# Kernel tuning notes

Measured on AMD Instinct MI355X. Metric: run time of the kernel, lower is better.

The kernel has to match this reference:

```python
import jax, jax.numpy as jnp
import numpy as np

B, S, H, KVH, D = 1, 2048, 32, 8, 128
ROPE_THETA = 500000.0


def _rotate_half(x):
    x1, x2 = jnp.split(x, 2, axis=-1)
    return jnp.concatenate((-x2, x1), axis=-1)


def setup_inputs() -> dict:
    key = jax.random.key(0)
    ks = jax.random.split(key, 5)
    hidden_states = jax.random.normal(ks[0], (B, S, H * D), dtype=jnp.float32)
    Wq = jax.random.normal(ks[1], (H * D, H * D), dtype=jnp.float32) * 0.02
    Wk = jax.random.normal(ks[2], (KVH * D, H * D), dtype=jnp.float32) * 0.02
    Wv = jax.random.normal(ks[3], (KVH * D, H * D), dtype=jnp.float32) * 0.02
    Wo = jax.random.normal(ks[4], (H * D, H * D), dtype=jnp.float32) * 0.02
    # rotary tables (Llama-style, concat of freqs with itself)
    inv_freq = 1.0 / (ROPE_THETA ** (jnp.arange(0, D, 2, dtype=jnp.float32) / D))
    freqs = jnp.arange(S, dtype=jnp.float32)[:, None] * inv_freq[None, :]  # [S, D/2]
    emb = jnp.concatenate((freqs, freqs), axis=-1)  # [S, D]
    cos = jnp.cos(emb)[None]  # [1, S, D]
    sin = jnp.sin(emb)[None]
    # additive causal mask, matching SDPA attn_mask semantics
    causal = jnp.tril(jnp.ones((S, S), dtype=bool))
    attention_mask = jnp.where(causal, 0.0, -1e9).astype(jnp.float32)[None, None]  # [1,1,S,S]
    return {"hidden_states": hidden_states, "attention_mask": attention_mask,
            "cos": cos, "sin": sin, "Wq": Wq, "Wk": Wk, "Wv": Wv, "Wo": Wo}


def reference(hidden_states, attention_mask, cos, sin, Wq, Wk, Wv, Wo):
    b, s, _ = hidden_states.shape
    d = cos.shape[-1]
    h = Wq.shape[0] // d
    kvh = Wk.shape[0] // d
    g = h // kvh  # GQA group size

    # fused QKV projection (nn.Linear: y = x @ W^T), then split heads -> [b, heads, s, d]
    q = jnp.einsum('bsi,oi->bso', hidden_states, Wq).reshape(b, s, h, d).transpose(0, 2, 1, 3)
    k = jnp.einsum('bsi,oi->bso', hidden_states, Wk).reshape(b, s, kvh, d).transpose(0, 2, 1, 3)
    v = jnp.einsum('bsi,oi->bso', hidden_states, Wv).reshape(b, s, kvh, d).transpose(0, 2, 1, 3)

    # rotary embedding (unsqueeze_dim=1)
    c = cos[:, None]  # [b,1,s,d]
    sn = sin[:, None]
    q = q * c + _rotate_half(q) * sn
    k = k * c + _rotate_half(k) * sn

    # GQA: view q as [b, kvh, g, s, d]; contract against un-repeated k/v
    qg = q.reshape(b, kvh, g, s, d)
    scale = 1.0 / jnp.sqrt(jnp.float32(d))
    scores = jnp.einsum('bkgsd,bktd->bkgst', qg, k) * scale  # [b,kvh,g,s,s]
    scores = scores + attention_mask[:, :, None]  # broadcast [b,1,1,s,s]
    probs = jax.nn.softmax(scores, axis=-1)
    attn = jnp.einsum('bkgst,bktd->bkgsd', probs, v)  # [b,kvh,g,s,d]

    attn = attn.reshape(b, h, s, d).transpose(0, 2, 1, 3).reshape(b, s, h * d)
    out = jnp.einsum('bso,po->bsp', attn, Wo)
    return out
```

## Files before the change

### kernel.cpp

```cpp
#include <hip/hip_runtime.h>
#include <hip/hip_bf16.h>

#define SEQ 2048
#define HD  128
#define NH  32
#define NKV 8
#define MODEL 4096
#define KVDIM 1024
#define QKVN 6144

typedef __attribute__((ext_vector_type(8))) short short8;
typedef __attribute__((ext_vector_type(4))) short short4v;
typedef __attribute__((ext_vector_type(4))) float float4v;

#define MFMA16(a, b, c) __builtin_amdgcn_mfma_f32_16x16x32_bf16(a, b, c, 0, 0, 0)

__device__ __forceinline__ short f2bf(float x) {
  unsigned u = __builtin_bit_cast(unsigned, x);
  u += 0x7fffu + ((u >> 16) & 1u);
  return (short)(u >> 16);
}
__device__ __forceinline__ float bf2f(short s) {
  unsigned u = ((unsigned)(unsigned short)s) << 16;
  return __builtin_bit_cast(float, u);
}

__device__ __forceinline__ void async_copy16(const void* g, void* l) {
  __builtin_amdgcn_global_load_lds((const __attribute__((address_space(1))) void*)g,
                                   (__attribute__((address_space(3))) void*)l, 16, 0, 0);
}

__global__ __launch_bounds__(256) void cast_bf16(const float* __restrict__ in,
                                                 short* __restrict__ out, int n) {
  int i = (blockIdx.x * 256 + threadIdx.x) * 4;
  if (i < n) {
    float4v v = *(const float4v*)(in + i);
    short4v o;
    o[0] = f2bf(v[0]); o[1] = f2bf(v[1]); o[2] = f2bf(v[2]); o[3] = f2bf(v[3]);
    *(short4v*)(out + i) = o;
  }
}

__device__ __forceinline__ void store_out(float* C, size_t idx, float v) { C[idx] = v; }
__device__ __forceinline__ void store_out(short* C, size_t idx, float v) { C[idx] = f2bf(v); }

template <int NI, typename OUT>
__global__ __launch_bounds__(512, 2) void gemm256v(const short* __restrict__ A,
                                                   const short* __restrict__ B,
                                                   OUT* __restrict__ C,
                                                   int M, int N, int K) {
  constexpr int BN = NI * 64;
  __shared__ __align__(16) short As[2][256 * 64];
  __shared__ __align__(16) short Bs[2][BN * 64];
  const int tid = threadIdx.x;
  const int lane = tid & 63, w = tid >> 6;
  const int col = lane & 15, quad = lane >> 4;
  const int wm = w >> 2, wn = w & 3;

  const int nbx = N / BN;
  int bid = blockIdx.x, nwg = gridDim.x;
  int swz = (nwg & 7) ? bid : ((bid & 7) * (nwg >> 3) + (bid >> 3));
  const int m0 = (swz / nbx) << 8;
  const int n0 = (swz % nbx) * BN;

  const int srow = tid >> 3;
  const int schunk = (tid & 7) ^ (srow & 7);
  const short* pA = A + (size_t)(m0 + srow) * K + schunk * 8;
  const short* pB = B + (size_t)(n0 + srow) * K + schunk * 8;
  const int ldst = tid * 8;

  const int sw = (col & 7) << 3;
  const int kof0 = (quad * 8) ^ sw;
  const int kof1 = (32 + quad * 8) ^ sw;
  const int ra = wm * 128, rb = wn * (NI * 16);

  float4v acc[8][NI] = {};
  const int iters = K >> 6;

#define SA(buf, rA, kt) async_copy16(pA + (size_t)(rA) * K + (kt), &As[buf][(rA) * 64 + ldst])
#define SB_(buf, rB, kt) async_copy16(pB + (size_t)(rB) * K + (kt), &Bs[buf][(rB) * 64 + ldst])

  SA(0, 0, 0);  SA(0, 128, 0);
  SB_(0, 0, 0); SB_(0, 64, 0);
  if constexpr (NI == 3) SB_(0, 128, 0);
  SA(0, 64, 0); SA(0, 192, 0);
  asm volatile("s_waitcnt vmcnt(2)" ::: "memory");
  __builtin_amdgcn_s_barrier();

  for (int t = 0; t < iters; ++t) {
    const int cb = t & 1, nb = cb ^ 1;
    const int kt = (t + 1) << 6;
    const bool pf = (t + 1 < iters);
    const short* a_ = As[cb];
    const short* b_ = Bs[cb];
    short8 bf[NI][2];
    short8 af[2][2];

#pragma unroll
    for (int j = 0; j < 2; ++j) {
      const short* rp = a_ + (ra + j * 16 + col) * 64;
      af[j][0] = *(const short8*)(rp + kof0);
      af[j][1] = *(const short8*)(rp + kof1);
    }
#pragma unroll
    for (int ni = 0; ni < NI; ++ni) {
      const short* rp = b_ + (rb + ni * 16 + col) * 64;
      bf[ni][0] = *(const short8*)(rp + kof0);
      bf[ni][1] = *(const short8*)(rp + kof1);
    }
    if (pf) { SA(nb, 0, kt); SA(nb, 128, kt); }
    __builtin_amdgcn_s_barrier();
    asm volatile("s_waitcnt lgkmcnt(0)" ::: "memory");
    __builtin_amdgcn_sched_barrier(0);
    __builtin_amdgcn_s_setprio(1);
#pragma unroll
    for (int j = 0; j < 2; ++j)
#pragma unroll
      for (int ni = 0; ni < NI; ++ni) {
        acc[j][ni] = MFMA16(af[j][0], bf[ni][0], acc[j][ni]);
        acc[j][ni] = MFMA16(af[j][1], bf[ni][1], acc[j][ni]);
      }
    __builtin_amdgcn_s_setprio(0);
    __builtin_amdgcn_s_barrier();

#pragma unroll
    for (int j = 0; j < 2; ++j) {
      const short* rp = a_ + (ra + (2 + j) * 16 + col) * 64;
      af[j][0] = *(const short8*)(rp + kof0);
      af[j][1] = *(const short8*)(rp + kof1);
    }
    if (pf) { SB_(nb, 0, kt); SB_(nb, 64, kt); }
    __builtin_amdgcn_s_barrier();
    asm volatile("s_waitcnt lgkmcnt(0)" ::: "memory");
    __builtin_amdgcn_sched_barrier(0);
    __builtin_amdgcn_s_setprio(1);
#pragma unroll
    for (int j = 0; j < 2; ++j)
#pragma unroll
      for (int ni = 0; ni < NI; ++ni) {
        acc[2 + j][ni] = MFMA16(af[j][0], bf[ni][0], acc[2 + j][ni]);
        acc[2 + j][ni] = MFMA16(af[j][1], bf[ni][1], acc[2 + j][ni]);
      }
    __builtin_amdgcn_s_setprio(0);
    if (pf) asm volatile("s_waitcnt vmcnt(4)" ::: "memory");
    else    asm volatile("s_waitcnt vmcnt(0)" ::: "memory");
    __builtin_amdgcn_s_barrier();

#pragma unroll
    for (int j = 0; j < 2; ++j) {
      const short* rp = a_ + (ra + (4 + j) * 16 + col) * 64;
      af[j][0] = *(const short8*)(rp + kof0);
      af[j][1] = *(const short8*)(rp + kof1);
    }
    if (pf) { if constexpr (NI == 3) SB_(nb, 128, kt); }
    __builtin_amdgcn_s_barrier();
    asm volatile("s_waitcnt lgkmcnt(0)" ::: "memory");
    __builtin_amdgcn_sched_barrier(0);
    __builtin_amdgcn_s_setprio(1);
#pragma unroll
    for (int j = 0; j < 2; ++j)
#pragma unroll
      for (int ni = 0; ni < NI; ++ni) {
        acc[4 + j][ni] = MFMA16(af[j][0], bf[ni][0], acc[4 + j][ni]);
        acc[4 + j][ni] = MFMA16(af[j][1], bf[ni][1], acc[4 + j][ni]);
      }
    __builtin_amdgcn_s_setprio(0);
    __builtin_amdgcn_s_barrier();

#pragma unroll
    for (int j = 0; j < 2; ++j) {
      const short* rp = a_ + (ra + (6 + j) * 16 + col) * 64;
      af[j][0] = *(const short8*)(rp + kof0);
      af[j][1] = *(const short8*)(rp + kof1);
    }
    if (pf) { SA(nb, 64, kt); SA(nb, 192, kt); }
    __builtin_amdgcn_s_barrier();
    asm volatile("s_waitcnt lgkmcnt(0)" ::: "memory");
    __builtin_amdgcn_sched_barrier(0);
    __builtin_amdgcn_s_setprio(1);
#pragma unroll
    for (int j = 0; j < 2; ++j)
#pragma unroll
      for (int ni = 0; ni < NI; ++ni) {
        acc[6 + j][ni] = MFMA16(af[j][0], bf[ni][0], acc[6 + j][ni]);
        acc[6 + j][ni] = MFMA16(af[j][1], bf[ni][1], acc[6 + j][ni]);
      }
    __builtin_amdgcn_s_setprio(0);
    if (pf) asm volatile("s_waitcnt vmcnt(2)" ::: "memory");
    __builtin_amdgcn_s_barrier();
  }
#undef SA
#undef SB_

#pragma unroll
  for (int mi = 0; mi < 8; ++mi)
#pragma unroll
    for (int ni = 0; ni < NI; ++ni)
#pragma unroll
      for (int r = 0; r < 4; ++r) {
        int row = m0 + ra + mi * 16 + quad * 4 + r;
        int cc  = n0 + rb + ni * 16 + col;
        store_out(C, (size_t)row * N + cc, acc[mi][ni][r]);
      }
}

__global__ __launch_bounds__(128) void rope_kernel(const short* __restrict__ qkv,
                                                   const float* __restrict__ cosp,
                                                   const float* __restrict__ sinp,
                                                   short* __restrict__ qb,
                                                   short* __restrict__ kb) {
  int s = blockIdx.x, head = blockIdx.y, d = threadIdx.x;
  float c  = cosp[s * HD + d];
  float sn = sinp[s * HD + d];
  if (head < NH) {
    const short* base = qkv + (size_t)s * QKVN + head * HD;
    float x = bf2f(base[d]);
    float rot = (d < 64) ? -bf2f(base[d + 64]) : bf2f(base[d - 64]);
    qb[((size_t)(head * SEQ + s)) * HD + d] = f2bf((x * c + rot * sn) * 0.08838834764831845f);
  } else {
    int hk = head - NH;
    const short* base = qkv + (size_t)s * QKVN + MODEL + hk * HD;
    float x = bf2f(base[d]);
    float rot = (d < 64) ? -bf2f(base[d + 64]) : bf2f(base[d - 64]);
    kb[((size_t)(hk * SEQ + s)) * HD + d] = f2bf(x * c + rot * sn);
  }
}

__global__ __launch_bounds__(256) void vtrans_kernel(const short* __restrict__ qkv,
                                                     short* __restrict__ vt) {
  __shared__ short tile[32][34];
  int kv = blockIdx.z;
  int d0 = blockIdx.x * 32, s0 = blockIdx.y * 32;
  int tx = threadIdx.x, ty = threadIdx.y;
#pragma unroll
  for (int j = 0; j < 32; j += 8)
    tile[ty + j][tx] = qkv[(size_t)(s0 + ty + j) * QKVN + MODEL + KVDIM + kv * HD + d0 + tx];
  __syncthreads();
#pragma unroll
  for (int j = 0; j < 32; j += 8)
    vt[((size_t)(kv * HD + d0 + ty + j)) * SEQ + s0 + tx] = tile[tx][ty + j];
}

#define FKT 32
#define KLD 136
#define VLD 40
#define PLD 40

__global__ __launch_bounds__(256, 3) void flash_attn(const short* __restrict__ qb_,
                                                     const short* __restrict__ kb,
                                                     const short* __restrict__ vt,
                                                     short* __restrict__ attn) {
  __shared__ __align__(16) short Ks[2][FKT * KLD];
  __shared__ __align__(16) short Vs[2][HD * VLD];
  __shared__ __align__(16) short Ps[4][32 * PLD];
  const int tid = threadIdx.x;
  const int w = tid >> 6, lane = tid & 63;
  const int col = lane & 15, quad = lane >> 4;
  const int h = blockIdx.x;
  const int kv = h >> 2;
  const int yp = (blockIdx.y < 8) ? (15 - (int)blockIdx.y) : ((int)blockIdx.y - 8);
  const int qB0 = yp * 128;
  const int q0w = qB0 + w * 32;
  const int ntiles = qB0 / FKT + 4;

  short8 ones;
#pragma unroll
  for (int i = 0; i < 8; i++) ones[i] = (short)0x3F80;

  short8 qf[2][4];
  const short* qbase = qb_ + ((size_t)(h * SEQ + q0w + col)) * HD;
#pragma unroll
  for (int rt = 0; rt < 2; rt++)
#pragma unroll
    for (int ks = 0; ks < 4; ks++)
      qf[rt][ks] = *(const short8*)(qbase + rt * 16 * HD + ks * 32 + quad * 8);

  float4v o[2][8] = {};
  float4v la[2] = {};

  const int kg_off = tid * 8;
  const int klds0  = (kg_off >> 7) * KLD + (kg_off & 127);
  const int vd     = tid >> 2;
  const int vkof   = (tid & 3) * 8;
  const size_t vrow0 = ((size_t)(kv * HD + vd)) * SEQ;
  const size_t vrow1 = ((size_t)(kv * HD + vd + 64)) * SEQ;
  const int vlds0 = vd * VLD + vkof;
  const short* kgbase = kb + ((size_t)kv * SEQ) * HD;

  short8 kr0, kr1, vr0, vr1;
  kr0 = *(const short8*)(kgbase + kg_off);
  kr1 = *(const short8*)(kgbase + 2048 + kg_off);
  vr0 = *(const short8*)(vt + vrow0 + vkof);
  vr1 = *(const short8*)(vt + vrow1 + vkof);
  *(short8*)&Ks[0][klds0]            = kr0;
  *(short8*)&Ks[0][klds0 + 16 * KLD] = kr1;
  *(short8*)&Vs[0][vlds0]            = vr0;
  *(short8*)&Vs[0][vlds0 + 64 * VLD] = vr1;
  __syncthreads();

  for (int kt = 0; kt < ntiles; kt++) {
    const int b = kt & 1;
    const int key0 = kt * FKT;
    if (kt + 1 < ntiles) {
      const int nk0 = key0 + FKT;
      const short* kg = kgbase + (size_t)nk0 * HD;
      kr0 = *(const short8*)(kg + kg_off);
      kr1 = *(const short8*)(kg + 2048 + kg_off);
      vr0 = *(const short8*)(vt + vrow0 + nk0 + vkof);
      vr1 = *(const short8*)(vt + vrow1 + nk0 + vkof);
    }
    if (key0 <= q0w + 31) {
      float4v sct[2][2] = {};
#pragma unroll
      for (int ks = 0; ks < 4; ks++) {
        short8 kf0 = *(const short8*)&Ks[b][col * KLD + ks * 32 + quad * 8];
        short8 kf1 = *(const short8*)&Ks[b][(16 + col) * KLD + ks * 32 + quad * 8];
        sct[0][0] = MFMA16(kf0, qf[0][ks], sct[0][0]);
        sct[0][1] = MFMA16(kf0, qf[1][ks], sct[0][1]);
        sct[1][0] = MFMA16(kf1, qf[0][ks], sct[1][0]);
        sct[1][1] = MFMA16(kf1, qf[1][ks], sct[1][1]);
      }
      short* pw = Ps[w];
#pragma unroll
      for (int rt = 0; rt < 2; rt++) {
        int qrow = q0w + rt * 16 + col;
#pragma unroll
        for (int kt2 = 0; kt2 < 2; kt2++) {
          int keyb = key0 + kt2 * 16 + quad * 4;
          short4v p;
#pragma unroll
          for (int r = 0; r < 4; r++) {
            float s = sct[kt2][rt][r];
            if (keyb + r > qrow) s = -INFINITY;
            p[r] = f2bf(__expf(s));
          }
          *(short4v*)&pw[(rt * 16 + col) * PLD + kt2 * 16 + quad * 4] = p;
        }
      }
      asm volatile("s_waitcnt lgkmcnt(0)" ::: "memory");
      short8 pf0 = *(const short8*)&pw[col * PLD + quad * 8];
      short8 pf1 = *(const short8*)&pw[(16 + col) * PLD + quad * 8];
      la[0] = MFMA16(ones, pf0, la[0]);
      la[1] = MFMA16(ones, pf1, la[1]);
#pragma unroll
      for (int nc = 0; nc < 8; nc++) {
        short8 vb = *(const short8*)&Vs[b][(nc * 16 + col) * VLD + quad * 8];
        o[0][nc] = MFMA16(vb, pf0, o[0][nc]);
        o[1][nc] = MFMA16(vb, pf1, o[1][nc]);
      }
    }
    if (kt + 1 < ntiles) {
      const int nb = 1 - b;
      *(short8*)&Ks[nb][klds0]            = kr0;
      *(short8*)&Ks[nb][klds0 + 16 * KLD] = kr1;
      *(short8*)&Vs[nb][vlds0]            = vr0;
      *(short8*)&Vs[nb][vlds0 + 64 * VLD] = vr1;
    }
    __syncthreads();
  }

#pragma unroll
  for (int rt = 0; rt < 2; rt++) {
    float inv = 1.0f / la[rt][0];
    size_t rowbase = (size_t)(q0w + rt * 16 + col) * MODEL + h * HD + quad * 4;
#pragma unroll
    for (int nc = 0; nc < 8; nc++) {
      short4v ov;
#pragma unroll
      for (int r = 0; r < 4; r++) ov[r] = f2bf(o[rt][nc][r] * inv);
      *(short4v*)(attn + rowbase + nc * 16) = ov;
    }
  }
}

extern "C" void kernel_launch(void* const* d_in, const int* in_sizes, int n_in,
                              void* d_out, int out_size, void* d_ws, size_t ws_size,
                              hipStream_t stream) {
  const float* hidden = (const float*)d_in[0];
  const float* cosp = (const float*)d_in[2];
  const float* sinp = (const float*)d_in[3];
  const float* Wq   = (const float*)d_in[4];
  const float* Wk   = (const float*)d_in[5];
  const float* Wv   = (const float*)d_in[6];
  const float* Wo   = (const float*)d_in[7];

  char* ws = (char*)d_ws;
  size_t off = 0;
  auto alloc = [&](size_t bytes) {
    char* p = ws + off;
    off += (bytes + 255) & ~(size_t)255;
    return p;
  };
  short* wq_bf = (short*)alloc((size_t)MODEL * MODEL * 2);
  short* wk_bf = (short*)alloc((size_t)KVDIM * MODEL * 2);
  short* wv_bf = (short*)alloc((size_t)KVDIM * MODEL * 2);
  short* wo_bf = (short*)alloc((size_t)MODEL * MODEL * 2);
  short* h_bf  = (short*)alloc((size_t)SEQ * MODEL * 2);
  short* qkv_bf = (short*)alloc((size_t)SEQ * QKVN * 2);
  short* k_bf  = (short*)alloc((size_t)NKV * SEQ * HD * 2);
  short* v_t   = (short*)alloc((size_t)NKV * HD * SEQ * 2);
  short* attn_bf = (short*)alloc((size_t)SEQ * MODEL * 2);
  short* q_bf    = h_bf;

  {
    int n;
    n = SEQ * MODEL;    cast_bf16<<<n / 1024, 256, 0, stream>>>(hidden, h_bf, n);
    n = MODEL * MODEL;  cast_bf16<<<n / 1024, 256, 0, stream>>>(Wq, wq_bf, n);
    n = KVDIM * MODEL;  cast_bf16<<<n / 1024, 256, 0, stream>>>(Wk, wk_bf, n);
    n = KVDIM * MODEL;  cast_bf16<<<n / 1024, 256, 0, stream>>>(Wv, wv_bf, n);
    n = MODEL * MODEL;  cast_bf16<<<n / 1024, 256, 0, stream>>>(Wo, wo_bf, n);
  }

  gemm256v<3, short><<<dim3((SEQ / 256) * (QKVN / 192)), 512, 0, stream>>>(
      h_bf, wq_bf, qkv_bf, SEQ, QKVN, MODEL);

  rope_kernel<<<dim3(SEQ, NH + NKV), 128, 0, stream>>>(qkv_bf, cosp, sinp, q_bf, k_bf);
  vtrans_kernel<<<dim3(HD / 32, SEQ / 32, NKV), dim3(32, 8), 0, stream>>>(qkv_bf, v_t);

  flash_attn<<<dim3(NH, SEQ / 128), 256, 0, stream>>>(q_bf, k_bf, v_t, attn_bf);

  gemm256v<2, float><<<dim3((SEQ / 256) * (MODEL / 128)), 512, 0, stream>>>(
      attn_bf, wo_bf, (float*)d_out, SEQ, MODEL, MODEL);
}
```

Before: 542.6 us.

## Fuse input casts, restructure GEMM phases, add 128x128 GEMM for output projection

```diff
diff --git a/kernel.cpp b/kernel.cpp
--- a/kernel.cpp
+++ b/kernel.cpp
@@ -30,22 +30,32 @@
                                    (__attribute__((address_space(3))) void*)l, 16, 0, 0);
 }
 
-__global__ __launch_bounds__(256) void cast_bf16(const float* __restrict__ in,
-                                                 short* __restrict__ out, int n) {
-  int i = (blockIdx.x * 256 + threadIdx.x) * 4;
-  if (i < n) {
-    float4v v = *(const float4v*)(in + i);
-    short4v o;
-    o[0] = f2bf(v[0]); o[1] = f2bf(v[1]); o[2] = f2bf(v[2]); o[3] = f2bf(v[3]);
-    *(short4v*)(out + i) = o;
-  }
+__global__ __launch_bounds__(256) void cast_fused(const float* __restrict__ wq,
+                                                  const float* __restrict__ wk,
+                                                  const float* __restrict__ wv,
+                                                  const float* __restrict__ wo,
+                                                  const float* __restrict__ hid,
+                                                  short* __restrict__ dst) {
+  int b = blockIdx.x;
+  const float* src;
+  int rbase, lblk;
+  if (b < 16384)      { src = wq;  rbase = 0;     lblk = b; }
+  else if (b < 20480) { src = wk;  rbase = 16384; lblk = b - 16384; }
+  else if (b < 24576) { src = wv;  rbase = 20480; lblk = b - 20480; }
+  else if (b < 40960) { src = wo;  rbase = 24576; lblk = b - 24576; }
+  else                { src = hid; rbase = 40960; lblk = b - 40960; }
+  size_t li = (size_t)lblk * 1024 + threadIdx.x * 4;
+  float4v v = *(const float4v*)(src + li);
+  short4v o;
+  o[0] = f2bf(v[0]); o[1] = f2bf(v[1]); o[2] = f2bf(v[2]); o[3] = f2bf(v[3]);
+  *(short4v*)(dst + (size_t)rbase * 1024 + li) = o;
 }
 
 __device__ __forceinline__ void store_out(float* C, size_t idx, float v) { C[idx] = v; }
 __device__ __forceinline__ void store_out(short* C, size_t idx, float v) { C[idx] = f2bf(v); }
 
 template <int NI, typename OUT>
-__global__ __launch_bounds__(512, 2) void gemm256v(const short* __restrict__ A,
+__global__ __launch_bounds__(512, 2) void gemm256t(const short* __restrict__ A,
                                                    const short* __restrict__ B,
                                                    OUT* __restrict__ C,
                                                    int M, int N, int K) {
@@ -94,10 +104,10 @@
     const short* a_ = As[cb];
     const short* b_ = Bs[cb];
     short8 bf[NI][2];
-    short8 af[2][2];
-
-#pragma unroll
-    for (int j = 0; j < 2; ++j) {
+    short8 af[4][2];
+
+#pragma unroll
+    for (int j = 0; j < 4; ++j) {
       const short* rp = a_ + (ra + j * 16 + col) * 64;
       af[j][0] = *(const short8*)(rp + kof0);
       af[j][1] = *(const short8*)(rp + kof1);
@@ -108,82 +118,43 @@
       bf[ni][0] = *(const short8*)(rp + kof0);
       bf[ni][1] = *(const short8*)(rp + kof1);
     }
-    if (pf) { SA(nb, 0, kt); SA(nb, 128, kt); }
+    if (pf) { SA(nb, 0, kt); SA(nb, 128, kt); SB_(nb, 0, kt); SB_(nb, 64, kt); }
     __builtin_amdgcn_s_barrier();
     asm volatile("s_waitcnt lgkmcnt(0)" ::: "memory");
     __builtin_amdgcn_sched_barrier(0);
     __builtin_amdgcn_s_setprio(1);
 #pragma unroll
-    for (int j = 0; j < 2; ++j)
+    for (int j = 0; j < 4; ++j)
 #pragma unroll
       for (int ni = 0; ni < NI; ++ni) {
         acc[j][ni] = MFMA16(af[j][0], bf[ni][0], acc[j][ni]);
         acc[j][ni] = MFMA16(af[j][1], bf[ni][1], acc[j][ni]);
       }
     __builtin_amdgcn_s_setprio(0);
+    if (pf) asm volatile("s_waitcnt vmcnt(4)" ::: "memory");
+    else    asm volatile("s_waitcnt vmcnt(0)" ::: "memory");
     __builtin_amdgcn_s_barrier();
 
 #pragma unroll
-    for (int j = 0; j < 2; ++j) {
-      const short* rp = a_ + (ra + (2 + j) * 16 + col) * 64;
+    for (int j = 0; j < 4; ++j) {
+      const short* rp = a_ + (ra + (4 + j) * 16 + col) * 64;
       af[j][0] = *(const short8*)(rp + kof0);
       af[j][1] = *(const short8*)(rp + kof1);
     }
-    if (pf) { SB_(nb, 0, kt); SB_(nb, 64, kt); }
+    if (pf) {
+      if constexpr (NI == 3) SB_(nb, 128, kt);
+      SA(nb, 64, kt); SA(nb, 192, kt);
+    }
     __builtin_amdgcn_s_barrier();
     asm volatile("s_waitcnt lgkmcnt(0)" ::: "memory");
     __builtin_amdgcn_sched_barrier(0);
     __builtin_amdgcn_s_setprio(1);
 #pragma unroll
-    for (int j = 0; j < 2; ++j)
-#pragma unroll
-      for (int ni = 0; ni < NI; ++ni) {
-        acc[2 + j][ni] = MFMA16(af[j][0], bf[ni][0], acc[2 + j][ni]);
-        acc[2 + j][ni] = MFMA16(af[j][1], bf[ni][1], acc[2 + j][ni]);
-      }
-    __builtin_amdgcn_s_setprio(0);
-    if (pf) asm volatile("s_waitcnt vmcnt(4)" ::: "memory");
-    else    asm volatile("s_waitcnt vmcnt(0)" ::: "memory");
-    __builtin_amdgcn_s_barrier();
-
-#pragma unroll
-    for (int j = 0; j < 2; ++j) {
-      const short* rp = a_ + (ra + (4 + j) * 16 + col) * 64;
-      af[j][0] = *(const short8*)(rp + kof0);
-      af[j][1] = *(const short8*)(rp + kof1);
-    }
-    if (pf) { if constexpr (NI == 3) SB_(nb, 128, kt); }
-    __builtin_amdgcn_s_barrier();
-    asm volatile("s_waitcnt lgkmcnt(0)" ::: "memory");
-    __builtin_amdgcn_sched_barrier(0);
-    __builtin_amdgcn_s_setprio(1);
-#pragma unroll
-    for (int j = 0; j < 2; ++j)
+    for (int j = 0; j < 4; ++j)
 #pragma unroll
       for (int ni = 0; ni < NI; ++ni) {
         acc[4 + j][ni] = MFMA16(af[j][0], bf[ni][0], acc[4 + j][ni]);
         acc[4 + j][ni] = MFMA16(af[j][1], bf[ni][1], acc[4 + j][ni]);
-      }
-    __builtin_amdgcn_s_setprio(0);
-    __builtin_amdgcn_s_barrier();
-
-#pragma unroll
-    for (int j = 0; j < 2; ++j) {
-      const short* rp = a_ + (ra + (6 + j) * 16 + col) * 64;
-      af[j][0] = *(const short8*)(rp + kof0);
-      af[j][1] = *(const short8*)(rp + kof1);
-    }
-    if (pf) { SA(nb, 64, kt); SA(nb, 192, kt); }
-    __builtin_amdgcn_s_barrier();
-    asm volatile("s_waitcnt lgkmcnt(0)" ::: "memory");
-    __builtin_amdgcn_sched_barrier(0);
-    __builtin_amdgcn_s_setprio(1);
-#pragma unroll
-    for (int j = 0; j < 2; ++j)
-#pragma unroll
-      for (int ni = 0; ni < NI; ++ni) {
-        acc[6 + j][ni] = MFMA16(af[j][0], bf[ni][0], acc[6 + j][ni]);
-        acc[6 + j][ni] = MFMA16(af[j][1], bf[ni][1], acc[6 + j][ni]);
       }
     __builtin_amdgcn_s_setprio(0);
     if (pf) asm volatile("s_waitcnt vmcnt(2)" ::: "memory");
@@ -200,6 +171,79 @@
       for (int r = 0; r < 4; ++r) {
         int row = m0 + ra + mi * 16 + quad * 4 + r;
         int cc  = n0 + rb + ni * 16 + col;
+        store_out(C, (size_t)row * N + cc, acc[mi][ni][r]);
+      }
+}
+
+#define BM 128
+#define BN 128
+#define BK 32
+
+template <typename OUT>
+__global__ __launch_bounds__(256) void gemm_nt(const short* __restrict__ A,
+                                               const short* __restrict__ B,
+                                               OUT* __restrict__ C,
+                                               int M, int N, int K) {
+  __shared__ __align__(16) short As[2][BM * BK];
+  __shared__ __align__(16) short Bs[2][BN * BK];
+  int t = threadIdx.x;
+  int w = t >> 6, lane = t & 63;
+  int col = lane & 15, quad = lane >> 4;
+  int m0 = blockIdx.y * BM, n0 = blockIdx.x * BN;
+  int wr = (w >> 1) * 64, wc = (w & 1) * 64;
+
+  int srow   = lane >> 2;
+  int schunk = (lane & 3) ^ ((lane >> 3) & 3);
+  const short* Ag0 = A + (size_t)(m0 + w * 32 + srow) * K + schunk * 8;
+  const short* Ag1 = Ag0 + (size_t)16 * K;
+  const short* Bg0 = B + (size_t)(n0 + w * 32 + srow) * K + schunk * 8;
+  const short* Bg1 = Bg0 + (size_t)16 * K;
+  const int wofs0 = (w * 32) * BK;
+  const int wofs1 = (w * 32 + 16) * BK;
+
+  int aswz = (quad ^ ((col >> 1) & 3)) * 8;
+
+  float4v acc[4][4] = {};
+
+  async_copy16(Ag0, &As[0][wofs0]);
+  async_copy16(Ag1, &As[0][wofs1]);
+  async_copy16(Bg0, &Bs[0][wofs0]);
+  async_copy16(Bg1, &Bs[0][wofs1]);
+  __syncthreads();
+
+  const int iters = K / BK;
+  for (int it = 0; it < iters; it++) {
+    const int cb = it & 1, nb = cb ^ 1;
+    if (it + 1 < iters) {
+      const int k0 = (it + 1) * BK;
+      async_copy16(Ag0 + k0, &As[nb][wofs0]);
+      async_copy16(Ag1 + k0, &As[nb][wofs1]);
+      async_copy16(Bg0 + k0, &Bs[nb][wofs0]);
+      async_copy16(Bg1 + k0, &Bs[nb][wofs1]);
+    }
+    short8 af[4], bfr[4];
+#pragma unroll
+    for (int i = 0; i < 4; i++)
+      af[i] = *(const short8*)&As[cb][(wr + i * 16 + col) * BK + aswz];
+#pragma unroll
+    for (int i = 0; i < 4; i++)
+      bfr[i] = *(const short8*)&Bs[cb][(wc + i * 16 + col) * BK + aswz];
+#pragma unroll
+    for (int mi = 0; mi < 4; mi++)
+#pragma unroll
+      for (int ni = 0; ni < 4; ni++)
+        acc[mi][ni] = MFMA16(af[mi], bfr[ni], acc[mi][ni]);
+    __syncthreads();
+  }
+
+#pragma unroll
+  for (int mi = 0; mi < 4; mi++)
+#pragma unroll
+    for (int ni = 0; ni < 4; ni++)
+#pragma unroll
+      for (int r = 0; r < 4; r++) {
+        int row = m0 + wr + mi * 16 + quad * 4 + r;
+        int cc  = n0 + wc + ni * 16 + col;
         store_out(C, (size_t)row * N + cc, acc[mi][ni][r]);
       }
 }
@@ -402,16 +446,9 @@
   short* attn_bf = (short*)alloc((size_t)SEQ * MODEL * 2);
   short* q_bf    = h_bf;
 
-  {
-    int n;
-    n = SEQ * MODEL;    cast_bf16<<<n / 1024, 256, 0, stream>>>(hidden, h_bf, n);
-    n = MODEL * MODEL;  cast_bf16<<<n / 1024, 256, 0, stream>>>(Wq, wq_bf, n);
-    n = KVDIM * MODEL;  cast_bf16<<<n / 1024, 256, 0, stream>>>(Wk, wk_bf, n);
-    n = KVDIM * MODEL;  cast_bf16<<<n / 1024, 256, 0, stream>>>(Wv, wv_bf, n);
-    n = MODEL * MODEL;  cast_bf16<<<n / 1024, 256, 0, stream>>>(Wo, wo_bf, n);
-  }
-
-  gemm256v<3, short><<<dim3((SEQ / 256) * (QKVN / 192)), 512, 0, stream>>>(
+  cast_fused<<<49152, 256, 0, stream>>>(Wq, Wk, Wv, Wo, hidden, wq_bf);
+
+  gemm256t<3, short><<<dim3((SEQ / 256) * (QKVN / 192)), 512, 0, stream>>>(
       h_bf, wq_bf, qkv_bf, SEQ, QKVN, MODEL);
 
   rope_kernel<<<dim3(SEQ, NH + NKV), 128, 0, stream>>>(qkv_bf, cosp, sinp, q_bf, k_bf);
@@ -419,6 +456,6 @@
 
   flash_attn<<<dim3(NH, SEQ / 128), 256, 0, stream>>>(q_bf, k_bf, v_t, attn_bf);
 
-  gemm256v<2, float><<<dim3((SEQ / 256) * (MODEL / 128)), 512, 0, stream>>>(
+  gemm_nt<float><<<dim3(MODEL / BN, SEQ / BM), 256, 0, stream>>>(
       attn_bf, wo_bf, (float*)d_out, SEQ, MODEL, MODEL);
 }
```

New measurement: 518.7 us. 1.05x faster.
